# Kernel optimization log

Measured on AMD Instinct MI355X. Metric: run time of the kernel, lower is better.

## Reference

```python
import jax, jax.numpy as jnp
import numpy as np

FEATURES = 1024
NUM_HEADS = 16
HEAD_DIM = FEATURES // NUM_HEADS


def _cinit(key, shape):
    # complex_xavier_init from the source: std = sqrt(1/(fan_in + fan_out))
    fan_in = int(np.prod(shape[:-1]))
    fan_out = shape[-1]
    std = np.sqrt(1.0 / (fan_in + fan_out)).astype(np.float32)
    return jax.random.normal(key, shape, dtype=jnp.float32) * std


def setup_inputs() -> dict:
    key = jax.random.key(0)
    ks = jax.random.split(key, 12)
    B, S, F = 2, 2048, FEATURES
    inp = {
        'x_r': jax.random.normal(ks[0], (B, S, F), dtype=jnp.float32),
        'x_i': jax.random.normal(ks[1], (B, S, F), dtype=jnp.float32),
        'mask': jnp.ones((B, S), dtype=jnp.float32),
    }
    names = ['q', 'k', 'v', 'o']
    for idx, n in enumerate(names):
        inp[f'W{n}_r'] = _cinit(ks[2 + 2 * idx], (F, F))
        inp[f'W{n}_i'] = _cinit(ks[3 + 2 * idx], (F, F))
        inp[f'b{n}_r'] = jnp.zeros((F,), dtype=jnp.float32)
        inp[f'b{n}_i'] = jnp.zeros((F,), dtype=jnp.float32)
    return inp


def _complex_linear(xr, xi, Wr, Wi, br, bi):
    # (xr + i xi) @ (Wr + i Wi) + (br + i bi)
    yr = xr @ Wr - xi @ Wi + br
    yi = xr @ Wi + xi @ Wr + bi
    return yr, yi


def reference(x_r, x_i, mask,
              Wq_r, Wq_i, bq_r, bq_i,
              Wk_r, Wk_i, bk_r, bk_i,
              Wv_r, Wv_i, bv_r, bv_i,
              Wo_r, Wo_i, bo_r, bo_i):
    B, S, F = x_r.shape
    H, D = NUM_HEADS, HEAD_DIM

    Qr, Qi = _complex_linear(x_r, x_i, Wq_r, Wq_i, bq_r, bq_i)
    Kr, Ki = _complex_linear(x_r, x_i, Wk_r, Wk_i, bk_r, bk_i)
    Vr, Vi = _complex_linear(x_r, x_i, Wv_r, Wv_i, bv_r, bv_i)

    def split_heads(t):  # [B,S,F] -> [B,H,S,D]
        return t.reshape(B, S, H, D).transpose(0, 2, 1, 3)

    Qr, Qi, Kr, Ki, Vr, Vi = map(split_heads, (Qr, Qi, Kr, Ki, Vr, Vi))

    scale = 1.0 / jnp.sqrt(jnp.float32(D))
    # Re(Q K^H) = Qr.Kr + Qi.Ki
    scores = (jnp.einsum('bhqd,bhkd->bhqk', Qr, Kr)
              + jnp.einsum('bhqd,bhkd->bhqk', Qi, Ki)) * scale
    scores = scores + (1.0 - mask[:, None, None, :]) * -1e9
    attn = jax.nn.softmax(scores, axis=-1)  # real-valued weights

    out_r = jnp.einsum('bhqk,bhkd->bhqd', attn, Vr)
    out_i = jnp.einsum('bhqk,bhkd->bhqd', attn, Vi)

    def merge_heads(t):  # [B,H,S,D] -> [B,S,F]
        return t.transpose(0, 2, 1, 3).reshape(B, S, F)

    out_r, out_i = merge_heads(out_r), merge_heads(out_i)
    out_r, out_i = _complex_linear(out_r, out_i, Wo_r, Wo_i, bo_r, bo_i)
    # stack real/imag parts: [2, B, S, F]
    return jnp.stack([out_r, out_i], axis=0)
```

## Files before the change

### kernel.cpp

```cpp
#include <hip/hip_runtime.h>
#include <hip/hip_bf16.h>

typedef unsigned short u16;
typedef unsigned int   u32;
typedef __attribute__((ext_vector_type(8))) short bf16x8;
typedef __attribute__((ext_vector_type(4))) float f32x4;

#define FDIM 1024
#define NH   16
#define HD   64
#define SEQ  2048

#define MFMA16 __builtin_amdgcn_mfma_f32_16x16x32_bf16

__device__ __forceinline__ u16 f2bf(float f) {
    __hip_bfloat16 h = __float2bfloat16(f);
    return *reinterpret_cast<u16*>(&h);
}

__device__ __forceinline__ void g2l16(const u16* g, u16* l) {
    __builtin_amdgcn_global_load_lds(
        (const __attribute__((address_space(1))) unsigned int*)g,
        (__attribute__((address_space(3))) unsigned int*)l,
        16, 0, 0);
}

__device__ __forceinline__ float exp2v(float x) {
    float d;
    asm("v_exp_f32 %0, %1" : "=v"(d) : "v"(x));
    return d;
}

__global__ __launch_bounds__(256)
void convert_x(const float* __restrict__ xr, const float* __restrict__ xi,
               u16* __restrict__ dr, u16* __restrict__ di)
{
    const long n4 = (long)2 * SEQ * FDIM / 4;
    for (long i = (long)blockIdx.x * blockDim.x + threadIdx.x; i < n4;
         i += (long)gridDim.x * blockDim.x) {
        float4 v = ((const float4*)xr)[i];
        ushort4 o;
        o.x = f2bf(v.x); o.y = f2bf(v.y); o.z = f2bf(v.z); o.w = f2bf(v.w);
        ((ushort4*)dr)[i] = o;
        v = ((const float4*)xi)[i];
        o.x = f2bf(v.x); o.y = f2bf(v.y); o.z = f2bf(v.z); o.w = f2bf(v.w);
        ((ushort4*)di)[i] = o;
    }
}

__global__ __launch_bounds__(256)
void convert_w(const float* __restrict__ W0, const float* __restrict__ W1,
               const float* __restrict__ W2, const float* __restrict__ W3,
               const float* __restrict__ W4, const float* __restrict__ W5,
               const float* __restrict__ W6, const float* __restrict__ W7,
               u16* __restrict__ wt_base)
{
    __shared__ u16 T[64][68];
    const int z = blockIdx.z;
    const float* W = (z == 0) ? W0 : (z == 1) ? W1 : (z == 2) ? W2 : (z == 3) ? W3
                   : (z == 4) ? W4 : (z == 5) ? W5 : (z == 6) ? W6 : W7;
    u16* Wt = wt_base + (long)z * FDIM * FDIM;
    const int n0 = blockIdx.x * 64, k0 = blockIdx.y * 64;
    const int tid = threadIdx.x;
    const int cr = tid & 15, rr = tid >> 4;
    #pragma unroll
    for (int p = 0; p < 4; p++) {
        const int k = p * 16 + rr;
        float4 v = *(const float4*)&W[(long)(k0 + k) * FDIM + n0 + cr * 4];
        T[k][cr*4 + 0] = f2bf(v.x); T[k][cr*4 + 1] = f2bf(v.y);
        T[k][cr*4 + 2] = f2bf(v.z); T[k][cr*4 + 3] = f2bf(v.w);
    }
    __syncthreads();
    #pragma unroll
    for (int p = 0; p < 4; p++) {
        const int n = p * 16 + rr;
        ushort4 o;
        o.x = T[cr*4 + 0][n]; o.y = T[cr*4 + 1][n];
        o.z = T[cr*4 + 2][n]; o.w = T[cr*4 + 3][n];
        *(ushort4*)&Wt[(long)(n0 + n) * FDIM + k0 + cr*4] = o;
    }
}

__global__ __launch_bounds__(256, 4)
void proj_bf16(const u16* __restrict__ Xr_g, const u16* __restrict__ Xi_g,
               const u16* __restrict__ Wt_base,
               const float* __restrict__ bqr, const float* __restrict__ bqi,
               const float* __restrict__ bkr, const float* __restrict__ bki,
               const float* __restrict__ bvr, const float* __restrict__ bvi,
               u16* __restrict__ ws)
{
    __shared__ u16 XsR[2][64 * 32], XsI[2][64 * 32];
    __shared__ u16 WsR[2][64 * 32], WsI[2][64 * 32];

    const int L   = blockIdx.x + (blockIdx.y << 4) + (blockIdx.z << 9);
    const int xcd = L & 7;
    const int qq  = L >> 3;
    const int y   = qq & 31;
    const int gg  = qq >> 5;
    const int gid = gg * 8 + xcd;
    const int x   = gid & 15;
    const int zz  = gid >> 4;
    const int t = zz % 3, b = zz / 3;

    const u16* xr = Xr_g + (long)b * SEQ * FDIM;
    const u16* xi = Xi_g + (long)b * SEQ * FDIM;
    const long WT = (long)FDIM * FDIM;
    const u16* wr = Wt_base + (long)(2 * t) * WT;
    const u16* wi = wr + WT;
    const float* br = (t == 0) ? bqr : (t == 1) ? bkr : bvr;
    const float* bi = (t == 0) ? bqi : (t == 1) ? bki : bvi;
    const long TS = (long)2 * SEQ * FDIM;
    u16* outR = ws + (long)(t * 2) * TS + (long)b * SEQ * FDIM;
    u16* outI = outR + TS;

    const int tid = threadIdx.x;
    const int n0  = x * 64;
    const int m0  = y * 64;

    const int lane = tid & 63;
    const int wv   = tid >> 6;
    const int mwo  = (wv >> 1) * 32;
    const int nwo  = (wv & 1) * 32;
    const int ml   = lane & 15;
    const int kg   = lane >> 4;

    const int lr = lane >> 2;
    const int xc = (((lane & 3) ^ (lr & 3)) * 8);
    const int rc = ((kg ^ (ml & 3)) * 8);

    f32x4 accr[2][2], acci[2][2];
    #pragma unroll
    for (int i = 0; i < 2; i++)
        #pragma unroll
        for (int j = 0; j < 2; j++) { accr[i][j] = (f32x4)(0.0f); acci[i][j] = (f32x4)(0.0f); }

    #define PSTAGE(bufi, kk)                                                     \
        do {                                                                     \
            const int rsx  = wv * 16;                                            \
            const int rowx = rsx + lr;                                           \
            g2l16(xr + (long)(m0 + rowx) * FDIM + (kk) + xc, &XsR[bufi][rsx * 32]); \
            g2l16(xi + (long)(m0 + rowx) * FDIM + (kk) + xc, &XsI[bufi][rsx * 32]); \
            g2l16(wr + (long)(n0 + rowx) * FDIM + (kk) + xc, &WsR[bufi][rsx * 32]); \
            g2l16(wi + (long)(n0 + rowx) * FDIM + (kk) + xc, &WsI[bufi][rsx * 32]); \
        } while (0)

    int buf = 0;
    PSTAGE(0, 0);
    __syncthreads();

    for (int k0 = 0; k0 < FDIM; k0 += 32) {
        if (k0 + 32 < FDIM) PSTAGE(buf ^ 1, k0 + 32);

        bf16x8 ar[2], ai[2], nai[2], brf[2], bif[2];
        #pragma unroll
        for (int i = 0; i < 2; i++) {
            ar[i] = *(const bf16x8*)&XsR[buf][(mwo + 16*i + ml) * 32 + rc];
            union { bf16x8 v; u32 w[4]; } u;
            u.v = *(const bf16x8*)&XsI[buf][(mwo + 16*i + ml) * 32 + rc];
            ai[i] = u.v;
            u.w[0] ^= 0x80008000u; u.w[1] ^= 0x80008000u;
            u.w[2] ^= 0x80008000u; u.w[3] ^= 0x80008000u;
            nai[i] = u.v;
        }
        #pragma unroll
        for (int j = 0; j < 2; j++) {
            brf[j] = *(const bf16x8*)&WsR[buf][(nwo + 16*j + ml) * 32 + rc];
            bif[j] = *(const bf16x8*)&WsI[buf][(nwo + 16*j + ml) * 32 + rc];
        }
        #pragma unroll
        for (int i = 0; i < 2; i++)
            #pragma unroll
            for (int j = 0; j < 2; j++) {
                accr[i][j] = MFMA16(ar[i],  brf[j], accr[i][j], 0, 0, 0);
                accr[i][j] = MFMA16(nai[i], bif[j], accr[i][j], 0, 0, 0);
                acci[i][j] = MFMA16(ar[i],  bif[j], acci[i][j], 0, 0, 0);
                acci[i][j] = MFMA16(ai[i],  brf[j], acci[i][j], 0, 0, 0);
            }

        __syncthreads();
        buf ^= 1;
    }
    #undef PSTAGE

    #pragma unroll
    for (int j = 0; j < 2; j++) {
        const int n = n0 + nwo + 16*j + ml;
        const int hh = n >> 6, d = n & 63;
        const float bre = br[n];
        const float bim = bi[n];
        #pragma unroll
        for (int i = 0; i < 2; i++) {
            const int mb = m0 + mwo + 16*i + kg*4;
            if (t < 2) {
                #pragma unroll
                for (int r = 0; r < 4; r++) {
                    const long addr = ((long)hh * SEQ + (mb + r)) * HD + d;
                    outR[addr] = f2bf(accr[i][j][r] + bre);
                    outI[addr] = f2bf(acci[i][j][r] + bim);
                }
            } else {
                const long addr = ((long)hh * HD + d) * SEQ + mb;
                ushort4 vr, vi;
                vr.x = f2bf(accr[i][j][0] + bre); vr.y = f2bf(accr[i][j][1] + bre);
                vr.z = f2bf(accr[i][j][2] + bre); vr.w = f2bf(accr[i][j][3] + bre);
                vi.x = f2bf(acci[i][j][0] + bim); vi.y = f2bf(acci[i][j][1] + bim);
                vi.z = f2bf(acci[i][j][2] + bim); vi.w = f2bf(acci[i][j][3] + bim);
                *(ushort4*)&outR[addr] = vr;
                *(ushort4*)&outI[addr] = vi;
            }
        }
    }
}

__global__ __launch_bounds__(256, 4)
void attn_mfma(const u16* __restrict__ Qr_g, const u16* __restrict__ Qi_g,
               const u16* __restrict__ Kr_g, const u16* __restrict__ Ki_g,
               const u16* __restrict__ Vtr_g, const u16* __restrict__ Vti_g,
               const float* __restrict__ mask_g,
               u16* __restrict__ Ar_g, u16* __restrict__ Ai_g)
{
    __shared__ u16 KT[64 * 128];
    __shared__ u16 VT[128 * 64];

    const int tid  = threadIdx.x;
    const int lane = tid & 63;
    const int wv   = tid >> 6;
    const int ml   = lane & 15;
    const int quad = lane >> 4;

    const int L   = blockIdx.x + (blockIdx.y << 5) + (blockIdx.z << 9);
    const int xcd = L & 7, qq = L >> 3;
    const int q0  = (qq & 31) * 64;
    const int g   = ((qq >> 5) << 3) | xcd;
    const int h   = g & 15;
    const int b   = g >> 4;
    const long hb  = ((long)b * NH + h) * SEQ * HD;
    const float* mask = mask_g + (long)b * SEQ;

    bf16x8 qf[4];
    {
        const long row = hb + (long)(q0 + wv*16 + ml) * HD;
        qf[0] = *(const bf16x8*)(Qr_g + row + quad*8);
        qf[1] = *(const bf16x8*)(Qr_g + row + 32 + quad*8);
        qf[2] = *(const bf16x8*)(Qi_g + row + quad*8);
        qf[3] = *(const bf16x8*)(Qi_g + row + 32 + quad*8);
    }

    const u16* srcK[4];
    #pragma unroll
    for (int ii = 0; ii < 4; ii++) {
        const int rk = wv*16 + ii*4 + (lane >> 4);
        const int c  = (lane & 15) ^ (rk & 7);
        srcK[ii] = ((c < 8) ? Kr_g : Ki_g) + hb + (long)rk * HD + (c & 7) * 8;
    }
    const u16* srcV[4];
    #pragma unroll
    for (int jj = 0; jj < 4; jj++) {
        const int dv = wv*32 + jj*8 + (lane >> 3);
        const int c  = (lane & 7) ^ (dv & 7);
        srcV[jj] = ((dv < 64) ? Vtr_g : Vti_g) + hb + (long)(dv & 63) * SEQ + c * 8;
    }

    #define STAGE()                                                             \
        do {                                                                    \
            _Pragma("unroll")                                                   \
            for (int ii = 0; ii < 4; ii++)                                      \
                g2l16(srcK[ii], &KT[(wv*16 + ii*4) * 128]);                     \
            _Pragma("unroll")                                                   \
            for (int jj = 0; jj < 4; jj++)                                      \
                g2l16(srcV[jj], &VT[(wv*32 + jj*8) * 64]);                      \
            _Pragma("unroll")                                                   \
            for (int ii = 0; ii < 4; ii++) srcK[ii] += 64 * HD;                 \
            _Pragma("unroll")                                                   \
            for (int jj = 0; jj < 4; jj++) srcV[jj] += 64;                      \
        } while (0)

    f32x4 oacc[8];
    #pragma unroll
    for (int nt = 0; nt < 8; nt++) oacc[nt] = (f32x4)(0.0f);
    float m_run = -3.0e38f;
    float l_run = 0.0f;
    const float SCALE2 = 0.125f * 1.44269504088896f;
    const float MC     = -1.44269504e9f;

    const int NT = SEQ / 64;
    for (int t = 0; t < NT; ++t) {
        if (t) __syncthreads();
        STAGE();

        f32x4 mrow[4];
        #pragma unroll
        for (int mt = 0; mt < 4; mt++)
            mrow[mt] = *(const f32x4*)(mask + t*64 + mt*16 + quad*4);

        __syncthreads();

        f32x4 sacc[4];
        #pragma unroll
        for (int mt = 0; mt < 4; mt++) sacc[mt] = (f32x4)(0.0f);
        __builtin_amdgcn_s_setprio(1);
        #pragma unroll
        for (int mt = 0; mt < 4; mt++)
            #pragma unroll
            for (int kc = 0; kc < 4; kc++) {
                const bf16x8 kf = *(const bf16x8*)
                    &KT[(mt*16 + ml) * 128 + (((kc*4 + quad) ^ (ml & 7)) * 8)];
                sacc[mt] = MFMA16(kf, qf[kc], sacc[mt], 0, 0, 0);
            }
        __builtin_amdgcn_s_setprio(0);

        asm volatile("s_barrier" ::: "memory");

        u16* Pb = (u16*)&KT[0];
        float sv[4][4];
        #pragma unroll
        for (int mt = 0; mt < 4; mt++)
            #pragma unroll
            for (int r = 0; r < 4; r++)
                sv[mt][r] = sacc[mt][r] * SCALE2 + (1.0f - mrow[mt][r]) * MC;

        float mA = fmaxf(fmaxf(sv[0][0], sv[0][1]), fmaxf(sv[0][2], sv[0][3]));
        float mB = fmaxf(fmaxf(sv[1][0], sv[1][1]), fmaxf(sv[1][2], sv[1][3]));
        float mC2 = fmaxf(fmaxf(sv[2][0], sv[2][1]), fmaxf(sv[2][2], sv[2][3]));
        float mD = fmaxf(fmaxf(sv[3][0], sv[3][1]), fmaxf(sv[3][2], sv[3][3]));
        float mx = fmaxf(fmaxf(mA, mB), fmaxf(mC2, mD));
        mx = fmaxf(mx, __shfl_xor(mx, 16));
        mx = fmaxf(mx, __shfl_xor(mx, 32));

        const int grow = __any(mx > m_run);
        float mn, al;
        if (grow) { mn = fmaxf(m_run, mx); al = exp2v(m_run - mn); }
        else      { mn = m_run;            al = 1.0f; }

        float p[4][4];
        #pragma unroll
        for (int mt = 0; mt < 4; mt++) {
            p[mt][0] = exp2v(sv[mt][0] - mn);
            p[mt][1] = exp2v(sv[mt][1] - mn);
            p[mt][2] = exp2v(sv[mt][2] - mn);
            p[mt][3] = exp2v(sv[mt][3] - mn);
        }
        const int qrow = wv*16 + ml;
        #pragma unroll
        for (int mt = 0; mt < 4; mt++) {
            ushort4 pb;
            pb.x = f2bf(p[mt][0]); pb.y = f2bf(p[mt][1]);
            pb.z = f2bf(p[mt][2]); pb.w = f2bf(p[mt][3]);
            *(ushort4*)&Pb[(long)qrow * 64
                           + (((mt*2 + (quad >> 1)) ^ (ml & 7)) * 8)
                           + (quad & 1) * 4] = pb;
        }
        float s0 = (p[0][0] + p[0][1]) + (p[0][2] + p[0][3]);
        float s1 = (p[1][0] + p[1][1]) + (p[1][2] + p[1][3]);
        float s2 = (p[2][0] + p[2][1]) + (p[2][2] + p[2][3]);
        float s3 = (p[3][0] + p[3][1]) + (p[3][2] + p[3][3]);
        float ps = (s0 + s1) + (s2 + s3);
        ps += __shfl_xor(ps, 16);
        ps += __shfl_xor(ps, 32);
        if (grow) {
            l_run = l_run * al + ps;
            f32x4 al4;
            #pragma unroll
            for (int r = 0; r < 4; r++)
                al4[r] = __shfl(al, quad*20 + r);
            #pragma unroll
            for (int nt = 0; nt < 8; nt++) oacc[nt] *= al4;
        } else {
            l_run += ps;
        }
        m_run = mn;

        __builtin_amdgcn_s_setprio(1);
        #pragma unroll
        for (int kc = 0; kc < 2; kc++) {
            const int pchunk = ((kc*4 + quad) ^ (ml & 7)) * 8;
            const bf16x8 pf = *(const bf16x8*)&Pb[(long)qrow * 64 + pchunk];
            #pragma unroll
            for (int nt = 0; nt < 8; nt++) {
                const bf16x8 vf = *(const bf16x8*)
                    &VT[(nt*16 + ml) * 64 + (((kc*4 + quad) ^ (ml & 7)) * 8)];
                oacc[nt] = MFMA16(pf, vf, oacc[nt], 0, 0, 0);
            }
        }
        __builtin_amdgcn_s_setprio(0);
    }
    #undef STAGE

    const float linv = 1.0f / l_run;
    f32x4 li;
    #pragma unroll
    for (int r = 0; r < 4; r++)
        li[r] = __shfl(linv, quad*20 + r);
    const long abase = (long)b * SEQ * FDIM;
    #pragma unroll
    for (int nt = 0; nt < 8; nt++) {
        const int dim = nt*16 + ml;
        u16* dst = ((dim < 64) ? Ar_g : Ai_g) + abase
                 + (long)(q0 + wv*16 + quad*4) * FDIM + h * HD + (dim & 63);
        #pragma unroll
        for (int r = 0; r < 4; r++)
            dst[(long)r * FDIM] = f2bf(oacc[nt][r] * li[r]);
    }
}

__global__ __launch_bounds__(256, 4)
void oproj_bf16(const u16* __restrict__ Ar_all, const u16* __restrict__ Ai_all,
                const u16* __restrict__ Wtor,
                const float* __restrict__ bor, const float* __restrict__ boi,
                float* __restrict__ out)
{
    __shared__ u16 XsR[2][64 * 32], XsI[2][64 * 32];
    __shared__ u16 WsR[2][64 * 32], WsI[2][64 * 32];

    const int L   = blockIdx.x + (blockIdx.y << 4) + (blockIdx.z << 9);
    const int xcd = L & 7;
    const int qq  = L >> 3;
    const int y   = qq & 31;
    const int gg  = qq >> 5;
    const int gid = gg * 8 + xcd;
    const int x   = gid & 15;
    const int b   = gid >> 4;

    const u16* ar = Ar_all + (long)b * SEQ * FDIM;
    const u16* ai = Ai_all + (long)b * SEQ * FDIM;
    const u16* wr = Wtor;
    const u16* wi = Wtor + (long)FDIM * FDIM;
    float* outR = out + (long)b * SEQ * FDIM;
    float* outI = out + (long)2 * SEQ * FDIM + (long)b * SEQ * FDIM;

    const int tid = threadIdx.x;
    const int n0  = x * 64;
    const int m0  = y * 64;

    const int lane = tid & 63;
    const int wv   = tid >> 6;
    const int mwo  = (wv >> 1) * 32;
    const int nwo  = (wv & 1) * 32;
    const int ml   = lane & 15;
    const int kg   = lane >> 4;

    const int lr = lane >> 2;
    const int xc = (((lane & 3) ^ (lr & 3)) * 8);
    const int rc = ((kg ^ (ml & 3)) * 8);

    f32x4 accr[2][2], acci[2][2];
    #pragma unroll
    for (int i = 0; i < 2; i++)
        #pragma unroll
        for (int j = 0; j < 2; j++) { accr[i][j] = (f32x4)(0.0f); acci[i][j] = (f32x4)(0.0f); }

    #define OSTAGE(bufi, kk)                                                     \
        do {                                                                     \
            const int rsx  = wv * 16;                                            \
            const int rowx = rsx + lr;                                           \
            g2l16(ar + (long)(m0 + rowx) * FDIM + (kk) + xc, &XsR[bufi][rsx * 32]); \
            g2l16(ai + (long)(m0 + rowx) * FDIM + (kk) + xc, &XsI[bufi][rsx * 32]); \
            g2l16(wr + (long)(n0 + rowx) * FDIM + (kk) + xc, &WsR[bufi][rsx * 32]); \
            g2l16(wi + (long)(n0 + rowx) * FDIM + (kk) + xc, &WsI[bufi][rsx * 32]); \
        } while (0)

    int buf = 0;
    OSTAGE(0, 0);
    __syncthreads();

    for (int k0 = 0; k0 < FDIM; k0 += 32) {
        if (k0 + 32 < FDIM) OSTAGE(buf ^ 1, k0 + 32);

        bf16x8 arf[2], aif[2], naif[2], brf[2], bif[2];
        #pragma unroll
        for (int i = 0; i < 2; i++) {
            arf[i] = *(const bf16x8*)&XsR[buf][(mwo + 16*i + ml) * 32 + rc];
            union { bf16x8 v; u32 w[4]; } u;
            u.v = *(const bf16x8*)&XsI[buf][(mwo + 16*i + ml) * 32 + rc];
            aif[i] = u.v;
            u.w[0] ^= 0x80008000u; u.w[1] ^= 0x80008000u;
            u.w[2] ^= 0x80008000u; u.w[3] ^= 0x80008000u;
            naif[i] = u.v;
        }
        #pragma unroll
        for (int j = 0; j < 2; j++) {
            brf[j] = *(const bf16x8*)&WsR[buf][(nwo + 16*j + ml) * 32 + rc];
            bif[j] = *(const bf16x8*)&WsI[buf][(nwo + 16*j + ml) * 32 + rc];
        }
        #pragma unroll
        for (int i = 0; i < 2; i++)
            #pragma unroll
            for (int j = 0; j < 2; j++) {
                accr[i][j] = MFMA16(arf[i],  brf[j], accr[i][j], 0, 0, 0);
                accr[i][j] = MFMA16(naif[i], bif[j], accr[i][j], 0, 0, 0);
                acci[i][j] = MFMA16(arf[i],  bif[j], acci[i][j], 0, 0, 0);
                acci[i][j] = MFMA16(aif[i],  brf[j], acci[i][j], 0, 0, 0);
            }

        __syncthreads();
        buf ^= 1;
    }
    #undef OSTAGE

    #pragma unroll
    for (int j = 0; j < 2; j++) {
        const int n = n0 + nwo + 16*j + ml;
        const float bre = bor[n];
        const float bim = boi[n];
        #pragma unroll
        for (int i = 0; i < 2; i++) {
            #pragma unroll
            for (int r = 0; r < 4; r++) {
                const int m = m0 + mwo + 16*i + kg*4 + r;
                const long addr = (long)m * FDIM + n;
                outR[addr] = accr[i][j][r] + bre;
                outI[addr] = acci[i][j][r] + bim;
            }
        }
    }
}

extern "C" void kernel_launch(void* const* d_in, const int* in_sizes, int n_in,
                              void* d_out, int out_size, void* d_ws, size_t ws_size,
                              hipStream_t stream)
{
    const float* x_r  = (const float*)d_in[0];
    const float* x_i  = (const float*)d_in[1];
    const float* mask = (const float*)d_in[2];
    const float *Wq_r = (const float*)d_in[3],  *Wq_i = (const float*)d_in[4];
    const float *bq_r = (const float*)d_in[5],  *bq_i = (const float*)d_in[6];
    const float *Wk_r = (const float*)d_in[7],  *Wk_i = (const float*)d_in[8];
    const float *bk_r = (const float*)d_in[9],  *bk_i = (const float*)d_in[10];
    const float *Wv_r = (const float*)d_in[11], *Wv_i = (const float*)d_in[12];
    const float *bv_r = (const float*)d_in[13], *bv_i = (const float*)d_in[14];
    const float *Wo_r = (const float*)d_in[15], *Wo_i = (const float*)d_in[16];
    const float *bo_r = (const float*)d_in[17], *bo_i = (const float*)d_in[18];

    u16* ws = (u16*)d_ws;
    const long TS = (long)2 * SEQ * FDIM;
    const long WT = (long)FDIM * FDIM;
    u16 *Qr = ws,          *Qi = ws + TS;
    u16 *Kr = ws + 2*TS,   *Ki = ws + 3*TS;
    u16 *Vtr = ws + 4*TS,  *Vti = ws + 5*TS;
    u16 *Ar = ws + 6*TS,   *Ai = ws + 7*TS;
    u16 *Xbr = Ar,         *Xbi = Ai;
    u16 *Wt  = ws + 8*TS;

    convert_x<<<dim3(2048), 256, 0, stream>>>(x_r, x_i, Xbr, Xbi);
    convert_w<<<dim3(16, 16, 8), 256, 0, stream>>>(Wq_r, Wq_i, Wk_r, Wk_i,
                                                   Wv_r, Wv_i, Wo_r, Wo_i, Wt);

    proj_bf16<<<dim3(16, 32, 6), 256, 0, stream>>>(Xbr, Xbi, Wt,
        bq_r, bq_i, bk_r, bk_i, bv_r, bv_i, ws);

    attn_mfma<<<dim3(SEQ / 64, NH, 2), 256, 0, stream>>>(Qr, Qi, Kr, Ki, Vtr, Vti,
                                                         mask, Ar, Ai);

    oproj_bf16<<<dim3(16, 32, 2), 256, 0, stream>>>(Ar, Ai, Wt + 6*WT,
                                                    bo_r, bo_i, (float*)d_out);
}
```

Before: 398.9 us.

## Replace double-buffered K=32 staging with single-buffered K=64 tiles in projections

Both projection GEMM kernels drop double buffering over K=32 slices and instead load a single 64-wide K tile per iteration, with a new 8-way XOR swizzle, then run two MFMA sub-steps per tile. This halves the number of loop iterations and barriers and keeps LDS use per block at 32 KB. Launch bounds go from 4 to 5 blocks per SM so more blocks can hide load latency, in place of software prefetch. The cost is that global-to-LDS loads no longer overlap compute within a block.

```diff
diff --git a/kernel.cpp b/kernel.cpp
--- a/kernel.cpp
+++ b/kernel.cpp
@@ -81,7 +81,7 @@
     }
 }
 
-__global__ __launch_bounds__(256, 4)
+__global__ __launch_bounds__(256, 5)
 void proj_bf16(const u16* __restrict__ Xr_g, const u16* __restrict__ Xi_g,
                const u16* __restrict__ Wt_base,
                const float* __restrict__ bqr, const float* __restrict__ bqi,
@@ -89,8 +89,8 @@
                const float* __restrict__ bvr, const float* __restrict__ bvi,
                u16* __restrict__ ws)
 {
-    __shared__ u16 XsR[2][64 * 32], XsI[2][64 * 32];
-    __shared__ u16 WsR[2][64 * 32], WsI[2][64 * 32];
+    __shared__ u16 XsR[64 * 64], XsI[64 * 64];
+    __shared__ u16 WsR[64 * 64], WsI[64 * 64];
 
     const int L   = blockIdx.x + (blockIdx.y << 4) + (blockIdx.z << 9);
     const int xcd = L & 7;
@@ -124,9 +124,8 @@
     const int ml   = lane & 15;
     const int kg   = lane >> 4;
 
-    const int lr = lane >> 2;
-    const int xc = (((lane & 3) ^ (lr & 3)) * 8);
-    const int rc = ((kg ^ (ml & 3)) * 8);
+    const int srow = wv*16 + (lane >> 3);
+    const int scol = (((lane & 7) ^ (lane >> 3)) * 8);
 
     f32x4 accr[2][2], acci[2][2];
     #pragma unroll
@@ -134,53 +133,54 @@
         #pragma unroll
         for (int j = 0; j < 2; j++) { accr[i][j] = (f32x4)(0.0f); acci[i][j] = (f32x4)(0.0f); }
 
-    #define PSTAGE(bufi, kk)                                                     \
-        do {                                                                     \
-            const int rsx  = wv * 16;                                            \
-            const int rowx = rsx + lr;                                           \
-            g2l16(xr + (long)(m0 + rowx) * FDIM + (kk) + xc, &XsR[bufi][rsx * 32]); \
-            g2l16(xi + (long)(m0 + rowx) * FDIM + (kk) + xc, &XsI[bufi][rsx * 32]); \
-            g2l16(wr + (long)(n0 + rowx) * FDIM + (kk) + xc, &WsR[bufi][rsx * 32]); \
-            g2l16(wi + (long)(n0 + rowx) * FDIM + (kk) + xc, &WsI[bufi][rsx * 32]); \
-        } while (0)
-
-    int buf = 0;
-    PSTAGE(0, 0);
-    __syncthreads();
-
-    for (int k0 = 0; k0 < FDIM; k0 += 32) {
-        if (k0 + 32 < FDIM) PSTAGE(buf ^ 1, k0 + 32);
-
-        bf16x8 ar[2], ai[2], nai[2], brf[2], bif[2];
-        #pragma unroll
-        for (int i = 0; i < 2; i++) {
-            ar[i] = *(const bf16x8*)&XsR[buf][(mwo + 16*i + ml) * 32 + rc];
-            union { bf16x8 v; u32 w[4]; } u;
-            u.v = *(const bf16x8*)&XsI[buf][(mwo + 16*i + ml) * 32 + rc];
-            ai[i] = u.v;
-            u.w[0] ^= 0x80008000u; u.w[1] ^= 0x80008000u;
-            u.w[2] ^= 0x80008000u; u.w[3] ^= 0x80008000u;
-            nai[i] = u.v;
-        }
-        #pragma unroll
-        for (int j = 0; j < 2; j++) {
-            brf[j] = *(const bf16x8*)&WsR[buf][(nwo + 16*j + ml) * 32 + rc];
-            bif[j] = *(const bf16x8*)&WsI[buf][(nwo + 16*j + ml) * 32 + rc];
-        }
-        #pragma unroll
-        for (int i = 0; i < 2; i++)
+    const long xoff = (long)(m0 + srow) * FDIM + scol;
+    const long woff = (long)(n0 + srow) * FDIM + scol;
+    const long r8   = (long)8 * FDIM;
+
+    for (int k0 = 0; k0 < FDIM; k0 += 64) {
+        if (k0) __syncthreads();
+        {
+            g2l16(xr + xoff + k0,      &XsR[(wv*16)     * 64]);
+            g2l16(xr + xoff + k0 + r8, &XsR[(wv*16 + 8) * 64]);
+            g2l16(xi + xoff + k0,      &XsI[(wv*16)     * 64]);
+            g2l16(xi + xoff + k0 + r8, &XsI[(wv*16 + 8) * 64]);
+            g2l16(wr + woff + k0,      &WsR[(wv*16)     * 64]);
+            g2l16(wr + woff + k0 + r8, &WsR[(wv*16 + 8) * 64]);
+            g2l16(wi + woff + k0,      &WsI[(wv*16)     * 64]);
+            g2l16(wi + woff + k0 + r8, &WsI[(wv*16 + 8) * 64]);
+        }
+        __syncthreads();
+
+        #pragma unroll
+        for (int kc = 0; kc < 2; kc++) {
+            const int rcc = (((kc*4 + kg) ^ (ml & 7)) * 8);
+            bf16x8 ar[2], ai[2], nai[2], brf[2], bif[2];
+            #pragma unroll
+            for (int i = 0; i < 2; i++) {
+                ar[i] = *(const bf16x8*)&XsR[(mwo + 16*i + ml) * 64 + rcc];
+                union { bf16x8 v; u32 w[4]; } u;
+                u.v = *(const bf16x8*)&XsI[(mwo + 16*i + ml) * 64 + rcc];
+                ai[i] = u.v;
+                u.w[0] ^= 0x80008000u; u.w[1] ^= 0x80008000u;
+                u.w[2] ^= 0x80008000u; u.w[3] ^= 0x80008000u;
+                nai[i] = u.v;
+            }
             #pragma unroll
             for (int j = 0; j < 2; j++) {
-                accr[i][j] = MFMA16(ar[i],  brf[j], accr[i][j], 0, 0, 0);
-                accr[i][j] = MFMA16(nai[i], bif[j], accr[i][j], 0, 0, 0);
-                acci[i][j] = MFMA16(ar[i],  bif[j], acci[i][j], 0, 0, 0);
-                acci[i][j] = MFMA16(ai[i],  brf[j], acci[i][j], 0, 0, 0);
-            }
-
-        __syncthreads();
-        buf ^= 1;
-    }
-    #undef PSTAGE
+                brf[j] = *(const bf16x8*)&WsR[(nwo + 16*j + ml) * 64 + rcc];
+                bif[j] = *(const bf16x8*)&WsI[(nwo + 16*j + ml) * 64 + rcc];
+            }
+            #pragma unroll
+            for (int i = 0; i < 2; i++)
+                #pragma unroll
+                for (int j = 0; j < 2; j++) {
+                    accr[i][j] = MFMA16(ar[i],  brf[j], accr[i][j], 0, 0, 0);
+                    accr[i][j] = MFMA16(nai[i], bif[j], accr[i][j], 0, 0, 0);
+                    acci[i][j] = MFMA16(ar[i],  bif[j], acci[i][j], 0, 0, 0);
+                    acci[i][j] = MFMA16(ai[i],  brf[j], acci[i][j], 0, 0, 0);
+                }
+        }
+    }
 
     #pragma unroll
     for (int j = 0; j < 2; j++) {
@@ -403,14 +403,14 @@
     }
 }
 
-__global__ __launch_bounds__(256, 4)
+__global__ __launch_bounds__(256, 5)
 void oproj_bf16(const u16* __restrict__ Ar_all, const u16* __restrict__ Ai_all,
                 const u16* __restrict__ Wtor,
                 const float* __restrict__ bor, const float* __restrict__ boi,
                 float* __restrict__ out)
 {
-    __shared__ u16 XsR[2][64 * 32], XsI[2][64 * 32];
-    __shared__ u16 WsR[2][64 * 32], WsI[2][64 * 32];
+    __shared__ u16 XsR[64 * 64], XsI[64 * 64];
+    __shared__ u16 WsR[64 * 64], WsI[64 * 64];
 
     const int L   = blockIdx.x + (blockIdx.y << 4) + (blockIdx.z << 9);
     const int xcd = L & 7;
@@ -439,9 +439,8 @@
     const int ml   = lane & 15;
     const int kg   = lane >> 4;
 
-    const int lr = lane >> 2;
-    const int xc = (((lane & 3) ^ (lr & 3)) * 8);
-    const int rc = ((kg ^ (ml & 3)) * 8);
+    const int srow = wv*16 + (lane >> 3);
+    const int scol = (((lane & 7) ^ (lane >> 3)) * 8);
 
     f32x4 accr[2][2], acci[2][2];
     #pragma unroll
@@ -449,53 +448,54 @@
         #pragma unroll
         for (int j = 0; j < 2; j++) { accr[i][j] = (f32x4)(0.0f); acci[i][j] = (f32x4)(0.0f); }
 
-    #define OSTAGE(bufi, kk)                                                     \
-        do {                                                                     \
-            const int rsx  = wv * 16;                                            \
-            const int rowx = rsx + lr;                                           \
-            g2l16(ar + (long)(m0 + rowx) * FDIM + (kk) + xc, &XsR[bufi][rsx * 32]); \
-            g2l16(ai + (long)(m0 + rowx) * FDIM + (kk) + xc, &XsI[bufi][rsx * 32]); \
-            g2l16(wr + (long)(n0 + rowx) * FDIM + (kk) + xc, &WsR[bufi][rsx * 32]); \
-            g2l16(wi + (long)(n0 + rowx) * FDIM + (kk) + xc, &WsI[bufi][rsx * 32]); \
-        } while (0)
-
-    int buf = 0;
-    OSTAGE(0, 0);
-    __syncthreads();
-
-    for (int k0 = 0; k0 < FDIM; k0 += 32) {
-        if (k0 + 32 < FDIM) OSTAGE(buf ^ 1, k0 + 32);
-
-        bf16x8 arf[2], aif[2], naif[2], brf[2], bif[2];
-        #pragma unroll
-        for (int i = 0; i < 2; i++) {
-            arf[i] = *(const bf16x8*)&XsR[buf][(mwo + 16*i + ml) * 32 + rc];
-            union { bf16x8 v; u32 w[4]; } u;
-            u.v = *(const bf16x8*)&XsI[buf][(mwo + 16*i + ml) * 32 + rc];
-            aif[i] = u.v;
-            u.w[0] ^= 0x80008000u; u.w[1] ^= 0x80008000u;
-            u.w[2] ^= 0x80008000u; u.w[3] ^= 0x80008000u;
-            naif[i] = u.v;
-        }
-        #pragma unroll
-        for (int j = 0; j < 2; j++) {
-            brf[j] = *(const bf16x8*)&WsR[buf][(nwo + 16*j + ml) * 32 + rc];
-            bif[j] = *(const bf16x8*)&WsI[buf][(nwo + 16*j + ml) * 32 + rc];
-        }
-        #pragma unroll
-        for (int i = 0; i < 2; i++)
+    const long xoff = (long)(m0 + srow) * FDIM + scol;
+    const long woff = (long)(n0 + srow) * FDIM + scol;
+    const long r8   = (long)8 * FDIM;
+
+    for (int k0 = 0; k0 < FDIM; k0 += 64) {
+        if (k0) __syncthreads();
+        {
+            g2l16(ar + xoff + k0,      &XsR[(wv*16)     * 64]);
+            g2l16(ar + xoff + k0 + r8, &XsR[(wv*16 + 8) * 64]);
+            g2l16(ai + xoff + k0,      &XsI[(wv*16)     * 64]);
+            g2l16(ai + xoff + k0 + r8, &XsI[(wv*16 + 8) * 64]);
+            g2l16(wr + woff + k0,      &WsR[(wv*16)     * 64]);
+            g2l16(wr + woff + k0 + r8, &WsR[(wv*16 + 8) * 64]);
+            g2l16(wi + woff + k0,      &WsI[(wv*16)     * 64]);
+            g2l16(wi + woff + k0 + r8, &WsI[(wv*16 + 8) * 64]);
+        }
+        __syncthreads();
+
+        #pragma unroll
+        for (int kc = 0; kc < 2; kc++) {
+            const int rcc = (((kc*4 + kg) ^ (ml & 7)) * 8);
+            bf16x8 arf[2], aif[2], naif[2], brf[2], bif[2];
+            #pragma unroll
+            for (int i = 0; i < 2; i++) {
+                arf[i] = *(const bf16x8*)&XsR[(mwo + 16*i + ml) * 64 + rcc];
+                union { bf16x8 v; u32 w[4]; } u;
+                u.v = *(const bf16x8*)&XsI[(mwo + 16*i + ml) * 64 + rcc];
+                aif[i] = u.v;
+                u.w[0] ^= 0x80008000u; u.w[1] ^= 0x80008000u;
+                u.w[2] ^= 0x80008000u; u.w[3] ^= 0x80008000u;
+                naif[i] = u.v;
+            }
             #pragma unroll
             for (int j = 0; j < 2; j++) {
-                accr[i][j] = MFMA16(arf[i],  brf[j], accr[i][j], 0, 0, 0);
-                accr[i][j] = MFMA16(naif[i], bif[j], accr[i][j], 0, 0, 0);
-                acci[i][j] = MFMA16(arf[i],  bif[j], acci[i][j], 0, 0, 0);
-                acci[i][j] = MFMA16(aif[i],  brf[j], acci[i][j], 0, 0, 0);
-            }
-
-        __syncthreads();
-        buf ^= 1;
-    }
-    #undef OSTAGE
+                brf[j] = *(const bf16x8*)&WsR[(nwo + 16*j + ml) * 64 + rcc];
+                bif[j] = *(const bf16x8*)&WsI[(nwo + 16*j + ml) * 64 + rcc];
+            }
+            #pragma unroll
+            for (int i = 0; i < 2; i++)
+                #pragma unroll
+                for (int j = 0; j < 2; j++) {
+                    accr[i][j] = MFMA16(arf[i],  brf[j], accr[i][j], 0, 0, 0);
+                    accr[i][j] = MFMA16(naif[i], bif[j], accr[i][j], 0, 0, 0);
+                    acci[i][j] = MFMA16(arf[i],  bif[j], acci[i][j], 0, 0, 0);
+                    acci[i][j] = MFMA16(aif[i],  brf[j], acci[i][j], 0, 0, 0);
+                }
+        }
+    }
 
     #pragma unroll
     for (int j = 0; j < 2; j++) {
```

After: 402.6 us. No clear change (+0.9%).
